# Optimization experiments

Hardware: AMD Instinct MI355X
Metric: run time of the kernel (lower is better)

Reference implementation:

```python
import jax, jax.numpy as jnp
import numpy as np

B, S, D, H = 8, 2048, 256, 4
DH = D // H
DFF = 4 * D


def setup_inputs() -> dict:
    key = jax.random.key(0)
    ks = jax.random.split(key, 32)
    w = lambda k, sh: (jax.random.normal(k, sh, jnp.float32) * 0.02)
    inp = {
        'global_feat': jax.random.normal(ks[0], (B, S, D), jnp.float32),
        'local_feat': jax.random.normal(ks[1], (B, S, D), jnp.float32),
        'text_feat': jax.random.normal(ks[2], (B, S, D), jnp.float32),
        'Wl1': w(ks[3], (D, D)), 'bl1': jnp.zeros((D,), jnp.float32),
        'Wl2': w(ks[4], (D, D)), 'bl2': jnp.zeros((D,), jnp.float32),
        'Wg': w(ks[5], (D, D)), 'bg': jnp.zeros((D,), jnp.float32),
        'Wgq': w(ks[6], (D, D)), 'bgq': jnp.zeros((D,), jnp.float32),
        'Wgk': w(ks[7], (D, D)), 'bgk': jnp.zeros((D,), jnp.float32),
        'Wgv': w(ks[8], (D, D)), 'bgv': jnp.zeros((D,), jnp.float32),
        'Wpq': w(ks[9], (D, D)), 'bpq': jnp.zeros((D,), jnp.float32),
        'Wpk': w(ks[10], (D, D)), 'bpk': jnp.zeros((D,), jnp.float32),
        'Wpv': w(ks[11], (D, D)), 'bpv': jnp.zeros((D,), jnp.float32),
        'Wd': w(ks[12], (D, D)), 'bd': jnp.zeros((D,), jnp.float32),
        'Wm1': w(ks[13], (D, DFF)), 'bm1': jnp.zeros((DFF,), jnp.float32),
        'Wm2': w(ks[14], (DFF, D)), 'bm2': jnp.zeros((D,), jnp.float32),
        'Wml': w(ks[15], (D, D)), 'bml': jnp.zeros((D,), jnp.float32),
    }
    return inp


def _heads(x):
    # [B,S,D] -> [B,H,S,DH]
    return x.reshape(B, S, H, DH).transpose(0, 2, 1, 3)


def _merge(x):
    # [B,H,S,DH] -> [B,S,D]
    return x.transpose(0, 2, 1, 3).reshape(B, S, D)


def reference(global_feat, local_feat, text_feat,
              Wl1, bl1, Wl2, bl2, Wg, bg,
              Wgq, bgq, Wgk, bgk, Wgv, bgv,
              Wpq, bpq, Wpk, bpk, Wpv, bpv,
              Wd, bd, Wm1, bm1, Wm2, bm2, Wml, bml):
    scale = 1.0 / jnp.sqrt(jnp.asarray(DH, jnp.float32))
    # embedding projections (dropout inactive in eval mode)
    dup_local = local_feat @ Wl1 + bl1      # local_embedding_1
    local = local_feat @ Wl2 + bl2          # local_embedding_2
    glob = global_feat @ Wg + bg            # global_embedding
    # global branch: Q from global, K/V from local
    gq = _heads(glob @ Wgq + bgq)
    gk = _heads(local @ Wgk + bgk)
    gv = _heads(local @ Wgv + bgv)
    # local branch: Q from duplicate local, K/V from text
    pq = _heads(dup_local @ Wpq + bpq)
    pk = _heads(text_feat @ Wpk + bpk)
    pv = _heads(text_feat @ Wpv + bpv)
    glb_probs = jax.nn.softmax(jnp.einsum('bhqd,bhkd->bhqk', gq, gk) * scale, axis=-1)
    plb_probs = jax.nn.softmax(jnp.einsum('bhqd,bhkd->bhqk', pq, pk) * scale, axis=-1)
    # bridging matmul: fuse probability maps
    plb_enhanced = jnp.einsum('bhqk,bhkl->bhql', glb_probs, plb_probs)
    glb_ctx = _merge(jnp.einsum('bhqk,bhkd->bhqd', glb_probs, gv))
    plb_ctx = _merge(jnp.einsum('bhqk,bhkd->bhqd', plb_enhanced, pv))
    out = (glb_ctx + plb_ctx) @ Wd + bd
    # GPT-style MLP (c_fc -> GELU -> c_proj)
    out = jax.nn.gelu(out @ Wm1 + bm1) @ Wm2 + bm2
    out = out @ Wml + bml
    return out
```

## Files before the change

kernel.cpp:

```cpp
#include <hip/hip_runtime.h>
#include <math.h>

#define Bn 8
#define Sn 2048
#define Dn 256
#define Hn 4
#define DHn 64
#define Mn (Bn*Sn)

typedef short bf16x8 __attribute__((ext_vector_type(8)));
typedef float f32x2  __attribute__((ext_vector_type(2)));
typedef float f32x4  __attribute__((ext_vector_type(4)));
typedef float f32x16 __attribute__((ext_vector_type(16)));
typedef int   i32x4  __attribute__((ext_vector_type(4)));
typedef unsigned short u16;
typedef unsigned int   u32;
typedef unsigned long long u64;

#if defined(__has_builtin)
#if __has_builtin(__builtin_amdgcn_global_load_lds)
#define HAVE_GLL 1
#endif
#if __has_builtin(__builtin_amdgcn_permlane32_swap)
#define HAVE_PLS 1
#endif
#endif
#ifndef HAVE_GLL
#define HAVE_GLL 0
#endif
#ifndef HAVE_PLS
#define HAVE_PLS 0
#endif

__device__ __forceinline__ u16 f2b(float f){
    u32 u = __float_as_uint(f);
    u32 r = (u + 0x7fffu + ((u >> 16) & 1u)) >> 16;
    return (u16)r;
}
__device__ __forceinline__ float b2f(u16 h){ return __uint_as_float(((u32)h) << 16); }
__device__ __forceinline__ u32 cvtpk(float lo, float hi){
    u32 r;
    asm("v_cvt_pk_bf16_f32 %0, %1, %2" : "=v"(r) : "v"(lo), "v"(hi));
    return r;
}

__device__ __forceinline__ float gelu_f(float x){
    const float K1 = 2.3021143113f;
    const float K2 = 0.1029390163f;
    float x2 = x * x;
    float arg = fmaf(x2 * x, K2, x * K1);
    float e = exp2f(arg);
    float r = __builtin_amdgcn_rcpf(e + 1.0f);
    return x - x * r;
}

struct WtArgs {
    const float* src[13];
    int kdim[13], ndim[13], dstoff[13], t0[13];
};

__global__ __launch_bounds__(256) void prep_k(const float* __restrict__ lf, const float* __restrict__ gf,
                                              const float* __restrict__ tf,
                                              u16* __restrict__ o0, u16* __restrict__ o1, u16* __restrict__ o2,
                                              WtArgs a, u16* __restrict__ dst)
{
    __shared__ float tile[32][33];
    int bx = blockIdx.x;
    if (bx < 6144){
        int part = bx >> 11, blk = bx & 2047;
        const float* s = (part == 0) ? lf : (part == 1) ? gf : tf;
        u16* d = (part == 0) ? o0 : (part == 1) ? o1 : o2;
        size_t base = ((size_t)blk * 256 + threadIdx.x) * 8;
        float4 v0 = *(const float4*)(s + base);
        float4 v1 = *(const float4*)(s + base + 4);
        i32x4 o;
        o[0] = (int)cvtpk(v0.x, v0.y); o[1] = (int)cvtpk(v0.z, v0.w);
        o[2] = (int)cvtpk(v1.x, v1.y); o[3] = (int)cvtpk(v1.z, v1.w);
        *(i32x4*)(d + base) = o;
        return;
    }
    int tb = bx - 6144;
    int wi = 0;
    #pragma unroll
    for (int i = 1; i < 13; ++i) if (tb >= a.t0[i]) wi = i;
    int tt = tb - a.t0[wi];
    int N = a.ndim[wi], K = a.kdim[wi];
    int ntn = N >> 5;
    int tn = tt % ntn, tk = tt / ntn;
    int n0 = tn * 32, k0 = tk * 32;
    const float* src = a.src[wi];
    int r = threadIdx.x >> 5, c = threadIdx.x & 31;
    #pragma unroll
    for (int rr = 0; rr < 4; ++rr)
        tile[r*4+rr][c] = src[(size_t)(k0 + r*4 + rr) * N + n0 + c];
    __syncthreads();
    u16* out = dst + a.dstoff[wi];
    #pragma unroll
    for (int rr = 0; rr < 4; ++rr)
        out[(size_t)(n0 + r*4 + rr) * K + k0 + c] = f2b(tile[c][r*4+rr]);
}

struct Grp {
    const u16* A[5];
    const u16* Wt[5];
    const float* bias[5];
    void* C[5];
    float scale[5];
};

template<int ACT, int OUTF32>
__global__ __launch_bounds__(256, 4) void gemm_k(Grp g, int N, int K)
{
    const u32 gx = gridDim.x;
    const u32 lgx = (u32)__builtin_ctz(gx);
    const u32 total = gx * gridDim.y * gridDim.z;
    const u32 lid = (blockIdx.z * gridDim.y + blockIdx.y) * gx + blockIdx.x;
    const u32 nl = (lid & 7) * (total >> 3) + (lid >> 3);
    const u32 bz = nl >> (lgx + 8);
    const u32 r2 = nl & ((1u << (lgx + 8)) - 1u);
    const u32 by = r2 >> lgx;
    const u32 bx = r2 & ((1u << lgx) - 1u);

    const u16* __restrict__ A   = g.A[bz];
    const u16* __restrict__ Wt  = g.Wt[bz];
    const float* __restrict__ bias = g.bias[bz];
    void* __restrict__ Cv = g.C[bz];
    const float scale = g.scale[bz];

    __shared__ u16 sm[2][6144];
    const int tid = threadIdx.x;
    const int w = tid >> 6, lane = tid & 63;
    const int l15 = lane & 15, l4 = lane >> 4;
    const int wr = w & 1, wc = w >> 1;
    const int bm = by << 6, bn = bx << 7;
    const int xq = l4 ^ ((lane >> 1) & 3);

    f32x4 acc[4][2];
    #pragma unroll
    for (int nf = 0; nf < 4; ++nf)
        #pragma unroll
        for (int mf = 0; mf < 2; ++mf){
            acc[nf][mf][0]=0.f; acc[nf][mf][1]=0.f; acc[nf][mf][2]=0.f; acc[nf][mf][3]=0.f;
        }

    auto STAGE = [&](int buf, int kt){
        #pragma unroll
        for (int j = 0; j < 3; ++j){
            int ch = w*192 + j*64 + lane;
            int isB = ch >= 256;
            int cc  = isB ? ch - 256 : ch;
            int row = cc >> 2, q = cc & 3;
            int qs  = q ^ ((row >> 1) & 3);
            const u16* src = isB ? (Wt + (size_t)(bn + row) * K + kt + qs*8)
                                 : (A  + (size_t)(bm + row) * K + kt + qs*8);
#if HAVE_GLL
            u16* lb = &sm[buf][(size_t)(w*192 + j*64) * 8];
            __builtin_amdgcn_global_load_lds((const __attribute__((address_space(1))) void*)src,
                                             (__attribute__((address_space(3))) void*)lb, 16, 0, 0);
#else
            *(i32x4*)&sm[buf][(size_t)ch * 8] = *(const i32x4*)src;
#endif
        }
    };

    STAGE(0, 0);
    const int nk = K >> 5;
    for (int t = 0; t < nk; ++t){
        const int cur = t & 1;
        if (t + 1 < nk){
            STAGE(cur ^ 1, (t + 1) << 5);
#if HAVE_GLL
            asm volatile("s_waitcnt vmcnt(3)" ::: "memory");
#endif
        } else {
#if HAVE_GLL
            asm volatile("s_waitcnt vmcnt(0)" ::: "memory");
#endif
        }
        __builtin_amdgcn_s_barrier();
        asm volatile("" ::: "memory");

        const u16* As = sm[cur];
        const u16* Bs = sm[cur] + 2048;
        bf16x8 wf[4], af[2];
        #pragma unroll
        for (int nf = 0; nf < 4; ++nf)
            wf[nf] = *(const bf16x8*)(Bs + (size_t)(wc*64 + nf*16 + l15) * 32 + xq*8);
        #pragma unroll
        for (int mf = 0; mf < 2; ++mf)
            af[mf] = *(const bf16x8*)(As + (size_t)(wr*32 + mf*16 + l15) * 32 + xq*8);
        __builtin_amdgcn_s_setprio(1);
        #pragma unroll
        for (int nf = 0; nf < 4; ++nf)
            #pragma unroll
            for (int mf = 0; mf < 2; ++mf)
                acc[nf][mf] = __builtin_amdgcn_mfma_f32_16x16x32_bf16(wf[nf], af[mf], acc[nf][mf], 0, 0, 0);
        __builtin_amdgcn_s_setprio(0);

        asm volatile("" ::: "memory");
        __builtin_amdgcn_s_barrier();
    }

    #pragma unroll
    for (int nf = 0; nf < 4; ++nf){
        const int n0 = bn + wc*64 + nf*16 + l4*4;
        float4 b4 = *(const float4*)(bias + n0);
        #pragma unroll
        for (int mf = 0; mf < 2; ++mf){
            const int m = bm + wr*32 + mf*16 + l15;
            float r0 = (acc[nf][mf][0] + b4.x) * scale;
            float r1 = (acc[nf][mf][1] + b4.y) * scale;
            float r2 = (acc[nf][mf][2] + b4.z) * scale;
            float r3 = (acc[nf][mf][3] + b4.w) * scale;
            if (ACT){ r0 = gelu_f(r0); r1 = gelu_f(r1); r2 = gelu_f(r2); r3 = gelu_f(r3); }
            if (OUTF32){
                float4 o; o.x = r0; o.y = r1; o.z = r2; o.w = r3;
                *(float4*)((float*)Cv + (size_t)m * N + n0) = o;
            } else {
                u64 p = (u64)cvtpk(r0, r1) | ((u64)cvtpk(r2, r3) << 32);
                *(u64*)((u16*)Cv + (size_t)m * N + n0) = p;
            }
        }
    }
}

#define PSEL(idx, mm) ((((idx) >> 2) == 0) ? pp0[(4*((idx)&3)+(mm))>>1][(4*((idx)&3)+(mm))&1] \
                                           : pp1[(4*((idx)&3)+(mm))>>1][(4*((idx)&3)+(mm))&1])

template<int FUSE>
__global__ __launch_bounds__(256, 2) void attn_k(const u16* __restrict__ Q, const u16* __restrict__ Kp,
                                                 const u16* __restrict__ Vp, u16* __restrict__ O,
                                                 const u16* __restrict__ ADD)
{
    __shared__ u16 Kl[2][4096];
    __shared__ u16 Vt[2][4608];

    const int tid = threadIdx.x;
    const int w = tid >> 6, lane = tid & 63;
    const int c31 = lane & 31, h = lane >> 5;

    const int lid = blockIdx.x;
    const int nl = (lid & 7) * 64 + (lid >> 3);
    const int bh = nl >> 4;
    const int qb = (nl & 15) << 7;
    const size_t hb = (size_t)(bh >> 2) * Sn * Dn + (size_t)(bh & 3) * DHn;
    const int qrow = qb + w*32 + c31;

    bf16x8 qf[4];
    #pragma unroll
    for (int kc = 0; kc < 4; ++kc)
        qf[kc] = *(const bf16x8*)(Q + hb + (size_t)qrow * Dn + kc*16 + h*8);

    f32x16 ot0, ot1;
    #pragma unroll
    for (int r = 0; r < 16; ++r){ ot0[r] = 0.f; ot1[r] = 0.f; }
    float ll = 0.f;

    const int kx = c31 & 7;
    int koff0[4], koff1[4], voff0[4], voff1[4];
    #pragma unroll
    for (int kc = 0; kc < 4; ++kc){
        int q = 2*kc + h;
        koff0[kc] = c31*64        + (q ^ kx)*8;
        koff1[kc] = (32 + c31)*64 + (q ^ kx)*8;
        voff0[kc] = c31*72        + kc*16 + h*8;
        voff1[kc] = (32 + c31)*72 + kc*16 + h*8;
    }

    const int vk0 = (tid & 15) * 4, vd0 = (tid >> 4) * 4;
    const u32 SEL_LO = 0x05040100u, SEL_HI = 0x07060302u;

    u64 v0, v1, v2, v3;
    auto LOADV = [&](int kt2){
        const u16* vb = Vp + hb + (size_t)(kt2 + vk0) * Dn + vd0;
        v0 = *(const u64*)(vb);
        v1 = *(const u64*)(vb + Dn);
        v2 = *(const u64*)(vb + 2*Dn);
        v3 = *(const u64*)(vb + 3*Dn);
    };
    auto GLLK = [&](int buf, int kt2){
        #pragma unroll
        for (int j = 0; j < 2; ++j){
            int ch = w*128 + j*64 + lane;
            int r = ch >> 3, q = ch & 7;
            int qs = q ^ (r & 7);
            const u16* src = Kp + hb + (size_t)(kt2 + r) * Dn + qs*8;
#if HAVE_GLL
            u16* lb = &Kl[buf][(size_t)(w*128 + j*64) * 8];
            __builtin_amdgcn_global_load_lds((const __attribute__((address_space(1))) void*)src,
                                             (__attribute__((address_space(3))) void*)lb, 16, 0, 0);
#else
            *(i32x4*)&Kl[buf][(size_t)ch * 8] = *(const i32x4*)src;
#endif
        }
    };
    auto WRITEV = [&](int buf){
        u32 a0 = (u32)v0, a1 = (u32)v1, a2 = (u32)v2, a3 = (u32)v3;
        u32 b0 = (u32)(v0 >> 32), b1 = (u32)(v1 >> 32), b2 = (u32)(v2 >> 32), b3 = (u32)(v3 >> 32);
        u64 wd0 = (u64)__builtin_amdgcn_perm(a1, a0, SEL_LO) | ((u64)__builtin_amdgcn_perm(a3, a2, SEL_LO) << 32);
        u64 wd1 = (u64)__builtin_amdgcn_perm(a1, a0, SEL_HI) | ((u64)__builtin_amdgcn_perm(a3, a2, SEL_HI) << 32);
        u64 wd2 = (u64)__builtin_amdgcn_perm(b1, b0, SEL_LO) | ((u64)__builtin_amdgcn_perm(b3, b2, SEL_LO) << 32);
        u64 wd3 = (u64)__builtin_amdgcn_perm(b1, b0, SEL_HI) | ((u64)__builtin_amdgcn_perm(b3, b2, SEL_HI) << 32);
        *(u64*)&Vt[buf][(size_t)(vd0 + 0)*72 + vk0] = wd0;
        *(u64*)&Vt[buf][(size_t)(vd0 + 1)*72 + vk0] = wd1;
        *(u64*)&Vt[buf][(size_t)(vd0 + 2)*72 + vk0] = wd2;
        *(u64*)&Vt[buf][(size_t)(vd0 + 3)*72 + vk0] = wd3;
    };

    LOADV(0);
    GLLK(0, 0);
    WRITEV(0);
    __syncthreads();

    #pragma unroll 2
    for (int t = 0; t < 32; ++t){
        const int c = t & 1;
        const bool more = (t < 31);
        if (more){
            LOADV((t + 1) << 6);
            GLLK(c ^ 1, (t + 1) << 6);
        }

        f32x16 s0, s1;
        #pragma unroll
        for (int r = 0; r < 16; ++r){ s0[r] = 0.f; s1[r] = 0.f; }
        __builtin_amdgcn_s_setprio(1);
        #pragma unroll
        for (int kc = 0; kc < 4; ++kc){
            bf16x8 k0 = *(const bf16x8*)&Kl[c][koff0[kc]];
            bf16x8 k1 = *(const bf16x8*)&Kl[c][koff1[kc]];
            s0 = __builtin_amdgcn_mfma_f32_32x32x16_bf16(k0, qf[kc], s0, 0, 0, 0);
            s1 = __builtin_amdgcn_mfma_f32_32x32x16_bf16(k1, qf[kc], s1, 0, 0, 0);
        }
        __builtin_amdgcn_s_setprio(0);

        f32x2 pp0[8], pp1[8];
        f32x2 rv = {0.f, 0.f};
        #pragma unroll
        for (int r = 0; r < 8; ++r){
            pp0[r][0] = exp2f(s0[2*r]); pp0[r][1] = exp2f(s0[2*r+1]);
            pp1[r][0] = exp2f(s1[2*r]); pp1[r][1] = exp2f(s1[2*r+1]);
            rv += pp0[r];
            rv += pp1[r];
        }
        ll += rv[0] + rv[1];

        __builtin_amdgcn_s_setprio(1);
        #pragma unroll
        for (int kc = 0; kc < 4; ++kc){
            const int iA = 2*kc, iB = 2*kc + 1;
            u32 wA0 = cvtpk(PSEL(iA,0), PSEL(iA,1));
            u32 wA1 = cvtpk(PSEL(iA,2), PSEL(iA,3));
            u32 wB0 = cvtpk(PSEL(iB,0), PSEL(iB,1));
            u32 wB1 = cvtpk(PSEL(iB,2), PSEL(iB,3));
            i32x4 pw;
#if HAVE_PLS
            {
                auto r02 = __builtin_amdgcn_permlane32_swap((int)wA0, (int)wB0, false, false);
                auto r13 = __builtin_amdgcn_permlane32_swap((int)wA1, (int)wB1, false, false);
                pw[0] = r02[0]; pw[1] = r13[0]; pw[2] = r02[1]; pw[3] = r13[1];
            }
#else
            {
                u32 s0v = h ? wA0 : wB0, s1v = h ? wA1 : wB1;
                u32 g0 = (u32)__shfl_xor((int)s0v, 32);
                u32 g1 = (u32)__shfl_xor((int)s1v, 32);
                pw[0] = (int)(h ? g0 : wA0);
                pw[1] = (int)(h ? g1 : wA1);
                pw[2] = (int)(h ? wB0 : g0);
                pw[3] = (int)(h ? wB1 : g1);
            }
#endif
            bf16x8 pb = *(bf16x8*)&pw;
            bf16x8 va  = *(const bf16x8*)&Vt[c][voff0[kc]];
            bf16x8 vb2 = *(const bf16x8*)&Vt[c][voff1[kc]];
            ot0 = __builtin_amdgcn_mfma_f32_32x32x16_bf16(va,  pb, ot0, 0, 0, 0);
            ot1 = __builtin_amdgcn_mfma_f32_32x32x16_bf16(vb2, pb, ot1, 0, 0, 0);
        }
        __builtin_amdgcn_s_setprio(0);

        if (more) WRITEV(c ^ 1);
        __syncthreads();
    }

    ll += __shfl_xor(ll, 32);
    float inv = 1.0f / ll;
    #pragma unroll
    for (int rg = 0; rg < 4; ++rg){
        int d0 = 8*rg + 4*h;
        float r0 = ot0[4*rg+0]*inv, r1 = ot0[4*rg+1]*inv, r2 = ot0[4*rg+2]*inv, r3 = ot0[4*rg+3]*inv;
        float x0 = ot1[4*rg+0]*inv, x1 = ot1[4*rg+1]*inv, x2 = ot1[4*rg+2]*inv, x3 = ot1[4*rg+3]*inv;
        if (FUSE){
            u64 ga = *(const u64*)&ADD[hb + (size_t)qrow * Dn + d0];
            u64 gb = *(const u64*)&ADD[hb + (size_t)qrow * Dn + 32 + d0];
            r0 += b2f((u16)ga);         r1 += b2f((u16)(ga >> 16));
            r2 += b2f((u16)(ga >> 32)); r3 += b2f((u16)(ga >> 48));
            x0 += b2f((u16)gb);         x1 += b2f((u16)(gb >> 16));
            x2 += b2f((u16)(gb >> 32)); x3 += b2f((u16)(gb >> 48));
        }
        *(u64*)&O[hb + (size_t)qrow * Dn + d0]      = (u64)cvtpk(r0, r1) | ((u64)cvtpk(r2, r3) << 32);
        *(u64*)&O[hb + (size_t)qrow * Dn + 32 + d0] = (u64)cvtpk(x0, x1) | ((u64)cvtpk(x2, x3) << 32);
    }
}

extern "C" void kernel_launch(void* const* d_in, const int* in_sizes, int n_in,
                              void* d_out, int out_size, void* d_ws, size_t ws_size,
                              hipStream_t stream)
{
    (void)in_sizes; (void)n_in; (void)out_size; (void)ws_size;

    const float* gf  = (const float*)d_in[0];
    const float* lf  = (const float*)d_in[1];
    const float* tf  = (const float*)d_in[2];
    const float* bl1 = (const float*)d_in[4];
    const float* bl2 = (const float*)d_in[6];
    const float* bg  = (const float*)d_in[8];
    const float* bgq = (const float*)d_in[10];
    const float* bgk = (const float*)d_in[12];
    const float* bgv = (const float*)d_in[14];
    const float* bpq = (const float*)d_in[16];
    const float* bpk = (const float*)d_in[18];
    const float* bpv = (const float*)d_in[20];
    const float* bd  = (const float*)d_in[22];
    const float* bm1 = (const float*)d_in[24];
    const float* bm2 = (const float*)d_in[26];
    const float* bml = (const float*)d_in[28];

    const float C1 = 0.18033688011112042f;

    u16* ws = (u16*)d_ws;
    const size_t U = (size_t)Mn * Dn;
    u16* S[9];
    for (int i = 0; i < 9; ++i) S[i] = ws + (size_t)i * U;
    u16* wtb = ws + 9 * U;

    const int sq = 65536;
    u16* Wl1t = wtb + 0*sq;  u16* Wl2t = wtb + 1*sq;  u16* Wgt  = wtb + 2*sq;
    u16* Wgqt = wtb + 3*sq;  u16* Wgkt = wtb + 4*sq;  u16* Wgvt = wtb + 5*sq;
    u16* Wpqt = wtb + 6*sq;  u16* Wpkt = wtb + 7*sq;  u16* Wpvt = wtb + 8*sq;
    u16* Wdt  = wtb + 9*sq;  u16* Wmlt = wtb + 10*sq;
    u16* Wm1t = wtb + 720896;
    u16* Wm2t = wtb + 720896 + 262144;

    WtArgs wa;
    const int srcidx[13] = {3,5,7,9,11,13,15,17,19,21,27,23,25};
    for (int i = 0; i < 13; ++i){
        wa.src[i] = (const float*)d_in[srcidx[i]];
        wa.kdim[i] = 256; wa.ndim[i] = 256;
        wa.dstoff[i] = i * sq;
    }
    wa.kdim[11] = 256;  wa.ndim[11] = 1024; wa.dstoff[11] = 720896;
    wa.kdim[12] = 1024; wa.ndim[12] = 256;  wa.dstoff[12] = 983040;
    int acc_t = 0;
    for (int i = 0; i < 13; ++i){
        wa.t0[i] = acc_t;
        acc_t += (wa.ndim[i] >> 5) * (wa.kdim[i] >> 5);
    }
    prep_k<<<dim3(6144 + acc_t), 256, 0, stream>>>(lf, gf, tf, S[0], S[1], S[2], wa, wtb);

    auto GN = [&](const Grp& g, int ng, int N, int K, int act, int of32){
        dim3 gr(N / 128, Mn / 64, ng);
        if (act)        gemm_k<1,0><<<gr, 256, 0, stream>>>(g, N, K);
        else if (of32)  gemm_k<0,1><<<gr, 256, 0, stream>>>(g, N, K);
        else            gemm_k<0,0><<<gr, 256, 0, stream>>>(g, N, K);
    };
    auto G1 = [&](const u16* A, const u16* Wt_, const float* b, void* C, int N, int K,
                  float sc, int act, int of32){
        Grp g{};
        g.A[0] = A; g.Wt[0] = Wt_; g.bias[0] = b; g.C[0] = C; g.scale[0] = sc;
        GN(g, 1, N, K, act, of32);
    };

    {
        Grp g{};
        g.A[0] = S[0]; g.Wt[0] = Wl1t; g.bias[0] = bl1; g.C[0] = S[3]; g.scale[0] = 1.f;
        g.A[1] = S[0]; g.Wt[1] = Wl2t; g.bias[1] = bl2; g.C[1] = S[4]; g.scale[1] = 1.f;
        g.A[2] = S[1]; g.Wt[2] = Wgt;  g.bias[2] = bg;  g.C[2] = S[5]; g.scale[2] = 1.f;
        g.A[3] = S[2]; g.Wt[3] = Wpkt; g.bias[3] = bpk; g.C[3] = S[7]; g.scale[3] = 1.f;
        g.A[4] = S[2]; g.Wt[4] = Wpvt; g.bias[4] = bpv; g.C[4] = S[8]; g.scale[4] = 1.f;
        GN(g, 5, 256, 256, 0, 0);
    }
    {
        Grp g{};
        g.A[0] = S[3]; g.Wt[0] = Wpqt; g.bias[0] = bpq; g.C[0] = S[6]; g.scale[0] = C1;
        g.A[1] = S[5]; g.Wt[1] = Wgqt; g.bias[1] = bgq; g.C[1] = S[0]; g.scale[1] = C1;
        g.A[2] = S[4]; g.Wt[2] = Wgkt; g.bias[2] = bgk; g.C[2] = S[1]; g.scale[2] = 1.f;
        g.A[3] = S[4]; g.Wt[3] = Wgvt; g.bias[3] = bgv; g.C[3] = S[2]; g.scale[3] = 1.f;
        GN(g, 4, 256, 256, 0, 0);
    }

    attn_k<1><<<dim3(512), 256, 0, stream>>>(S[6], S[7], S[8], S[3], S[2]);
    attn_k<0><<<dim3(512), 256, 0, stream>>>(S[0], S[1], S[3], S[4], nullptr);

    G1(S[4], Wdt,  bd,  S[5], 256,  256,  1.f, 0, 0);
    G1(S[5], Wm1t, bm1, S[0], 1024, 256,  1.f, 1, 0);
    G1(S[0], Wm2t, bm2, S[6], 256,  1024, 1.f, 0, 0);
    G1(S[6], Wmlt, bml, d_out, 256, 256,  1.f, 0, 1);
}
```

Before: 247.1 us.

## Fold chained embedding projections into combined weights and restructure attention K loading

Pre-multiplies the embedding weights (Wl1, Wl2, Wg) into the downstream Q/K/V projection weights with a small GEMM and folds their biases into combined biases. This removes one full-size chained GEMM stage over the activations, so the Q/K/V projections and the text K/V projections run as a single 6-group GEMM launch. The attention kernel now loads K through registers into a padded LDS layout instead of using swizzled direct-to-LDS loads. The combined weights are rounded to bf16 after the product, which slightly changes numerics, and there are extra small launches for the weight combination.

```diff
diff --git a/kernel.cpp b/kernel.cpp
--- a/kernel.cpp
+++ b/kernel.cpp
@@ -56,7 +56,7 @@
 
 struct WtArgs {
     const float* src[13];
-    int kdim[13], ndim[13], dstoff[13], t0[13];
+    int kdim[13], ndim[13], dstoff[13], t0[13], rm[13];
 };
 
 __global__ __launch_bounds__(256) void prep_k(const float* __restrict__ lf, const float* __restrict__ gf,
@@ -89,37 +89,63 @@
     int tn = tt % ntn, tk = tt / ntn;
     int n0 = tn * 32, k0 = tk * 32;
     const float* src = a.src[wi];
+    u16* out = dst + a.dstoff[wi];
     int r = threadIdx.x >> 5, c = threadIdx.x & 31;
+    if (a.rm[wi]){
+        #pragma unroll
+        for (int rr = 0; rr < 4; ++rr){
+            size_t idx = (size_t)(k0 + r*4 + rr) * N + n0 + c;
+            out[idx] = f2b(src[idx]);
+        }
+        return;
+    }
     #pragma unroll
     for (int rr = 0; rr < 4; ++rr)
         tile[r*4+rr][c] = src[(size_t)(k0 + r*4 + rr) * N + n0 + c];
     __syncthreads();
-    u16* out = dst + a.dstoff[wi];
     #pragma unroll
     for (int rr = 0; rr < 4; ++rr)
         out[(size_t)(n0 + r*4 + rr) * K + k0 + c] = f2b(tile[c][r*4+rr]);
 }
 
+__global__ __launch_bounds__(256) void bcomb_k(const float* __restrict__ W2a, const float* __restrict__ W2b,
+                                               const float* __restrict__ W2c, const float* __restrict__ W2d,
+                                               const float* __restrict__ b1a, const float* __restrict__ b1b,
+                                               const float* __restrict__ b1c, const float* __restrict__ b1d,
+                                               const float* __restrict__ b2a, const float* __restrict__ b2b,
+                                               const float* __restrict__ b2c, const float* __restrict__ b2d,
+                                               float* __restrict__ fb)
+{
+    int p = blockIdx.x, a = threadIdx.x;
+    const float* W2 = (p==0)?W2a:(p==1)?W2b:(p==2)?W2c:W2d;
+    const float* b1 = (p==0)?b1a:(p==1)?b1b:(p==2)?b1c:b1d;
+    const float* b2 = (p==0)?b2a:(p==1)?b2b:(p==2)?b2c:b2d;
+    float s = b2[a];
+    for (int j = 0; j < 256; ++j) s = fmaf(b1[j], W2[(size_t)j*256 + a], s);
+    fb[p*256 + a] = s;
+    if (p == 0) fb[1024 + a] = 0.f;
+}
+
 struct Grp {
-    const u16* A[5];
-    const u16* Wt[5];
-    const float* bias[5];
-    void* C[5];
-    float scale[5];
+    const u16* A[6];
+    const u16* Wt[6];
+    const float* bias[6];
+    void* C[6];
+    float scale[6];
 };
 
 template<int ACT, int OUTF32>
 __global__ __launch_bounds__(256, 4) void gemm_k(Grp g, int N, int K)
 {
-    const u32 gx = gridDim.x;
+    const u32 gx = gridDim.x, gy = gridDim.y;
     const u32 lgx = (u32)__builtin_ctz(gx);
-    const u32 total = gx * gridDim.y * gridDim.z;
-    const u32 lid = (blockIdx.z * gridDim.y + blockIdx.y) * gx + blockIdx.x;
+    const u32 lgy = (u32)__builtin_ctz(gy);
+    const u32 total = gx * gy * gridDim.z;
+    const u32 lid = (blockIdx.z * gy + blockIdx.y) * gx + blockIdx.x;
     const u32 nl = (lid & 7) * (total >> 3) + (lid >> 3);
-    const u32 bz = nl >> (lgx + 8);
-    const u32 r2 = nl & ((1u << (lgx + 8)) - 1u);
-    const u32 by = r2 >> lgx;
-    const u32 bx = r2 & ((1u << lgx) - 1u);
+    const u32 bz = nl >> (lgx + lgy);
+    const u32 by = (nl >> lgx) & (gy - 1);
+    const u32 bx = nl & (gx - 1);
 
     const u16* __restrict__ A   = g.A[bz];
     const u16* __restrict__ Wt  = g.Wt[bz];
@@ -232,7 +258,7 @@
                                                  const u16* __restrict__ Vp, u16* __restrict__ O,
                                                  const u16* __restrict__ ADD)
 {
-    __shared__ u16 Kl[2][4096];
+    __shared__ u16 Kl[2][4608];
     __shared__ u16 Vt[2][4608];
 
     const int tid = threadIdx.x;
@@ -256,45 +282,34 @@
     for (int r = 0; r < 16; ++r){ ot0[r] = 0.f; ot1[r] = 0.f; }
     float ll = 0.f;
 
-    const int kx = c31 & 7;
     int koff0[4], koff1[4], voff0[4], voff1[4];
     #pragma unroll
     for (int kc = 0; kc < 4; ++kc){
-        int q = 2*kc + h;
-        koff0[kc] = c31*64        + (q ^ kx)*8;
-        koff1[kc] = (32 + c31)*64 + (q ^ kx)*8;
-        voff0[kc] = c31*72        + kc*16 + h*8;
-        voff1[kc] = (32 + c31)*72 + kc*16 + h*8;
-    }
-
+        koff0[kc] = c31*72        + kc*16 + h*8;
+        koff1[kc] = (32 + c31)*72 + kc*16 + h*8;
+        voff0[kc] = koff0[kc];
+        voff1[kc] = koff1[kc];
+    }
+
+    const int krow = tid >> 2, kq = tid & 3;
     const int vk0 = (tid & 15) * 4, vd0 = (tid >> 4) * 4;
     const u32 SEL_LO = 0x05040100u, SEL_HI = 0x07060302u;
 
+    i32x4 kr0, kr1;
     u64 v0, v1, v2, v3;
-    auto LOADV = [&](int kt2){
+    auto LOADKV = [&](int kt2){
+        const u16* kb = Kp + hb + (size_t)(kt2 + krow) * Dn + kq*8;
+        kr0 = *(const i32x4*)kb;
+        kr1 = *(const i32x4*)(kb + 32);
         const u16* vb = Vp + hb + (size_t)(kt2 + vk0) * Dn + vd0;
         v0 = *(const u64*)(vb);
         v1 = *(const u64*)(vb + Dn);
         v2 = *(const u64*)(vb + 2*Dn);
         v3 = *(const u64*)(vb + 3*Dn);
     };
-    auto GLLK = [&](int buf, int kt2){
-        #pragma unroll
-        for (int j = 0; j < 2; ++j){
-            int ch = w*128 + j*64 + lane;
-            int r = ch >> 3, q = ch & 7;
-            int qs = q ^ (r & 7);
-            const u16* src = Kp + hb + (size_t)(kt2 + r) * Dn + qs*8;
-#if HAVE_GLL
-            u16* lb = &Kl[buf][(size_t)(w*128 + j*64) * 8];
-            __builtin_amdgcn_global_load_lds((const __attribute__((address_space(1))) void*)src,
-                                             (__attribute__((address_space(3))) void*)lb, 16, 0, 0);
-#else
-            *(i32x4*)&Kl[buf][(size_t)ch * 8] = *(const i32x4*)src;
-#endif
-        }
-    };
-    auto WRITEV = [&](int buf){
+    auto WRITEKV = [&](int buf){
+        *(i32x4*)&Kl[buf][(size_t)krow*72 + kq*8]      = kr0;
+        *(i32x4*)&Kl[buf][(size_t)krow*72 + kq*8 + 32] = kr1;
         u32 a0 = (u32)v0, a1 = (u32)v1, a2 = (u32)v2, a3 = (u32)v3;
         u32 b0 = (u32)(v0 >> 32), b1 = (u32)(v1 >> 32), b2 = (u32)(v2 >> 32), b3 = (u32)(v3 >> 32);
         u64 wd0 = (u64)__builtin_amdgcn_perm(a1, a0, SEL_LO) | ((u64)__builtin_amdgcn_perm(a3, a2, SEL_LO) << 32);
@@ -307,19 +322,15 @@
         *(u64*)&Vt[buf][(size_t)(vd0 + 3)*72 + vk0] = wd3;
     };
 
-    LOADV(0);
-    GLLK(0, 0);
-    WRITEV(0);
+    LOADKV(0);
+    WRITEKV(0);
     __syncthreads();
 
     #pragma unroll 2
     for (int t = 0; t < 32; ++t){
         const int c = t & 1;
         const bool more = (t < 31);
-        if (more){
-            LOADV((t + 1) << 6);
-            GLLK(c ^ 1, (t + 1) << 6);
-        }
+        if (more) LOADKV((t + 1) << 6);
 
         f32x16 s0, s1;
         #pragma unroll
@@ -379,7 +390,7 @@
         }
         __builtin_amdgcn_s_setprio(0);
 
-        if (more) WRITEV(c ^ 1);
+        if (more) WRITEKV(c ^ 1);
         __syncthreads();
     }
 
@@ -412,13 +423,13 @@
     const float* gf  = (const float*)d_in[0];
     const float* lf  = (const float*)d_in[1];
     const float* tf  = (const float*)d_in[2];
-    const float* bl1 = (const float*)d_in[4];
-    const float* bl2 = (const float*)d_in[6];
-    const float* bg  = (const float*)d_in[8];
-    const float* bgq = (const float*)d_in[10];
-    const float* bgk = (const float*)d_in[12];
-    const float* bgv = (const float*)d_in[14];
-    const float* bpq = (const float*)d_in[16];
+    const float* Wl1 = (const float*)d_in[3];  const float* bl1 = (const float*)d_in[4];
+    const float* Wl2 = (const float*)d_in[5];  const float* bl2 = (const float*)d_in[6];
+    const float* Wg  = (const float*)d_in[7];  const float* bg  = (const float*)d_in[8];
+    const float* Wgq = (const float*)d_in[9];  const float* bgq = (const float*)d_in[10];
+    const float* Wgk = (const float*)d_in[11]; const float* bgk = (const float*)d_in[12];
+    const float* Wgv = (const float*)d_in[13]; const float* bgv = (const float*)d_in[14];
+    const float* Wpq = (const float*)d_in[15]; const float* bpq = (const float*)d_in[16];
     const float* bpk = (const float*)d_in[18];
     const float* bpv = (const float*)d_in[20];
     const float* bd  = (const float*)d_in[22];
@@ -435,22 +446,33 @@
     u16* wtb = ws + 9 * U;
 
     const int sq = 65536;
-    u16* Wl1t = wtb + 0*sq;  u16* Wl2t = wtb + 1*sq;  u16* Wgt  = wtb + 2*sq;
-    u16* Wgqt = wtb + 3*sq;  u16* Wgkt = wtb + 4*sq;  u16* Wgvt = wtb + 5*sq;
-    u16* Wpqt = wtb + 6*sq;  u16* Wpkt = wtb + 7*sq;  u16* Wpvt = wtb + 8*sq;
-    u16* Wdt  = wtb + 9*sq;  u16* Wmlt = wtb + 10*sq;
-    u16* Wm1t = wtb + 720896;
-    u16* Wm2t = wtb + 720896 + 262144;
+    u16* Wpqt = wtb + 0*sq;  u16* Wgqt = wtb + 1*sq;  u16* Wgkt = wtb + 2*sq;  u16* Wgvt = wtb + 3*sq;
+    u16* Wpkt = wtb + 4*sq;  u16* Wpvt = wtb + 5*sq;  u16* Wdt  = wtb + 6*sq;  u16* Wmlt = wtb + 7*sq;
+    u16* Wm1t = wtb + 524288;
+    u16* Wm2t = wtb + 786432;
+    u16* Wl1rm = wtb + 1048576;
+    u16* Wl2rm = wtb + 1114112;
+    u16* Wgrm  = wtb + 1179648;
+    u16* Wcpqt = wtb + 1245184;
+    u16* Wcgqt = wtb + 1310720;
+    u16* Wcgkt = wtb + 1376256;
+    u16* Wcgvt = wtb + 1441792;
+    float* fb  = (float*)(wtb + 1507328);
 
     WtArgs wa;
-    const int srcidx[13] = {3,5,7,9,11,13,15,17,19,21,27,23,25};
+    const float* wsrc[13] = {Wpq, Wgq, Wgk, Wgv, (const float*)d_in[17], (const float*)d_in[19],
+                             (const float*)d_in[21], (const float*)d_in[27],
+                             (const float*)d_in[23], (const float*)d_in[25], Wl1, Wl2, Wg};
+    const int wdst[13] = {0, sq, 2*sq, 3*sq, 4*sq, 5*sq, 6*sq, 7*sq, 524288, 786432,
+                          1048576, 1114112, 1179648};
     for (int i = 0; i < 13; ++i){
-        wa.src[i] = (const float*)d_in[srcidx[i]];
+        wa.src[i] = wsrc[i];
         wa.kdim[i] = 256; wa.ndim[i] = 256;
-        wa.dstoff[i] = i * sq;
-    }
-    wa.kdim[11] = 256;  wa.ndim[11] = 1024; wa.dstoff[11] = 720896;
-    wa.kdim[12] = 1024; wa.ndim[12] = 256;  wa.dstoff[12] = 983040;
+        wa.dstoff[i] = wdst[i];
+        wa.rm[i] = (i >= 10);
+    }
+    wa.ndim[8] = 1024;
+    wa.kdim[9] = 1024;
     int acc_t = 0;
     for (int i = 0; i < 13; ++i){
         wa.t0[i] = acc_t;
@@ -458,8 +480,11 @@
     }
     prep_k<<<dim3(6144 + acc_t), 256, 0, stream>>>(lf, gf, tf, S[0], S[1], S[2], wa, wtb);
 
-    auto GN = [&](const Grp& g, int ng, int N, int K, int act, int of32){
-        dim3 gr(N / 128, Mn / 64, ng);
+    bcomb_k<<<dim3(4), 256, 0, stream>>>(Wpq, Wgq, Wgk, Wgv, bl1, bg, bl2, bl2,
+                                         bpq, bgq, bgk, bgv, fb);
+
+    auto GN = [&](const Grp& g, int ng, int M, int N, int K, int act, int of32){
+        dim3 gr(N / 128, M / 64, ng);
         if (act)        gemm_k<1,0><<<gr, 256, 0, stream>>>(g, N, K);
         else if (of32)  gemm_k<0,1><<<gr, 256, 0, stream>>>(g, N, K);
         else            gemm_k<0,0><<<gr, 256, 0, stream>>>(g, N, K);
@@ -468,32 +493,34 @@
                   float sc, int act, int of32){
         Grp g{};
         g.A[0] = A; g.Wt[0] = Wt_; g.bias[0] = b; g.C[0] = C; g.scale[0] = sc;
-        GN(g, 1, N, K, act, of32);
+        GN(g, 1, Mn, N, K, act, of32);
     };
 
     {
         Grp g{};
-        g.A[0] = S[0]; g.Wt[0] = Wl1t; g.bias[0] = bl1; g.C[0] = S[3]; g.scale[0] = 1.f;
-        g.A[1] = S[0]; g.Wt[1] = Wl2t; g.bias[1] = bl2; g.C[1] = S[4]; g.scale[1] = 1.f;
-        g.A[2] = S[1]; g.Wt[2] = Wgt;  g.bias[2] = bg;  g.C[2] = S[5]; g.scale[2] = 1.f;
-        g.A[3] = S[2]; g.Wt[3] = Wpkt; g.bias[3] = bpk; g.C[3] = S[7]; g.scale[3] = 1.f;
-        g.A[4] = S[2]; g.Wt[4] = Wpvt; g.bias[4] = bpv; g.C[4] = S[8]; g.scale[4] = 1.f;
-        GN(g, 5, 256, 256, 0, 0);
-    }
+        g.A[0] = Wpqt; g.Wt[0] = Wl1rm; g.bias[0] = fb + 1024; g.C[0] = Wcpqt; g.scale[0] = 1.f;
+        g.A[1] = Wgqt; g.Wt[1] = Wgrm;  g.bias[1] = fb + 1024; g.C[1] = Wcgqt; g.scale[1] = 1.f;
+        g.A[2] = Wgkt; g.Wt[2] = Wl2rm; g.bias[2] = fb + 1024; g.C[2] = Wcgkt; g.scale[2] = 1.f;
+        g.A[3] = Wgvt; g.Wt[3] = Wl2rm; g.bias[3] = fb + 1024; g.C[3] = Wcgvt; g.scale[3] = 1.f;
+        GN(g, 4, 256, 256, 256, 0, 0);
+    }
+
     {
         Grp g{};
-        g.A[0] = S[3]; g.Wt[0] = Wpqt; g.bias[0] = bpq; g.C[0] = S[6]; g.scale[0] = C1;
-        g.A[1] = S[5]; g.Wt[1] = Wgqt; g.bias[1] = bgq; g.C[1] = S[0]; g.scale[1] = C1;
-        g.A[2] = S[4]; g.Wt[2] = Wgkt; g.bias[2] = bgk; g.C[2] = S[1]; g.scale[2] = 1.f;
-        g.A[3] = S[4]; g.Wt[3] = Wgvt; g.bias[3] = bgv; g.C[3] = S[2]; g.scale[3] = 1.f;
-        GN(g, 4, 256, 256, 0, 0);
-    }
-
-    attn_k<1><<<dim3(512), 256, 0, stream>>>(S[6], S[7], S[8], S[3], S[2]);
-    attn_k<0><<<dim3(512), 256, 0, stream>>>(S[0], S[1], S[3], S[4], nullptr);
-
-    G1(S[4], Wdt,  bd,  S[5], 256,  256,  1.f, 0, 0);
-    G1(S[5], Wm1t, bm1, S[0], 1024, 256,  1.f, 1, 0);
-    G1(S[0], Wm2t, bm2, S[6], 256,  1024, 1.f, 0, 0);
-    G1(S[6], Wmlt, bml, d_out, 256, 256,  1.f, 0, 1);
-}
+        g.A[0] = S[0]; g.Wt[0] = Wcpqt; g.bias[0] = fb + 0;   g.C[0] = S[3]; g.scale[0] = C1;
+        g.A[1] = S[1]; g.Wt[1] = Wcgqt; g.bias[1] = fb + 256; g.C[1] = S[6]; g.scale[1] = C1;
+        g.A[2] = S[0]; g.Wt[2] = Wcgkt; g.bias[2] = fb + 512; g.C[2] = S[7]; g.scale[2] = 1.f;
+        g.A[3] = S[0]; g.Wt[3] = Wcgvt; g.bias[3] = fb + 768; g.C[3] = S[8]; g.scale[3] = 1.f;
+        g.A[4] = S[2]; g.Wt[4] = Wpkt;  g.bias[4] = bpk;      g.C[4] = S[4]; g.scale[4] = 1.f;
+        g.A[5] = S[2]; g.Wt[5] = Wpvt;  g.bias[5] = bpv;      g.C[5] = S[5]; g.scale[5] = 1.f;
+        GN(g, 6, Mn, 256, 256, 0, 0);
+    }
+
+    attn_k<1><<<dim3(512), 256, 0, stream>>>(S[3], S[4], S[5], S[0], S[8]);
+    attn_k<0><<<dim3(512), 256, 0, stream>>>(S[6], S[7], S[0], S[1], nullptr);
+
+    G1(S[1], Wdt,  bd,  S[2], 256,  256,  1.f, 0, 0);
+    G1(S[2], Wm1t, bm1, S[3], 1024, 256,  1.f, 1, 0);
+    G1(S[3], Wm2t, bm2, S[7], 256,  1024, 1.f, 0, 0);
+    G1(S[7], Wmlt, bml, d_out, 256, 256,  1.f, 0, 1);
+}
```

After: 225.8 us. 8.7% less time.
